# Kernel optimization log

Hardware: AMD Instinct MI355X
Metric: run time of the kernel (lower is better)

Reference implementation:

```python
import jax, jax.numpy as jnp
import numpy as np

B, S, D, H = 4, 2048, 1024, 16
HD = D // H  # head dim = 64

def setup_inputs() -> dict:
    key = jax.random.key(0)
    ks = jax.random.split(key, 6)
    scale = 0.02
    x = jax.random.normal(ks[0], (B, S, D), dtype=jnp.float32)
    Wq = jax.random.normal(ks[1], (D, D), dtype=jnp.float32) * scale
    Wk = jax.random.normal(ks[2], (D, D), dtype=jnp.float32) * scale
    Wv = jax.random.normal(ks[3], (D, D), dtype=jnp.float32) * scale
    Wo = jax.random.normal(ks[4], (D, D), dtype=jnp.float32) * scale
    bo = jnp.zeros((D,), dtype=jnp.float32)
    return {"x": x, "Wq": Wq, "Wk": Wk, "Wv": Wv, "Wo": Wo, "bo": bo}

def reference(x, Wq, Wk, Wv, Wo, bo):
    b, s, d = x.shape
    h, hd = H, HD
    # project and split heads -> [b, h, s, hd]
    def split_heads(t):
        return t.reshape(b, s, h, hd).transpose(0, 2, 1, 3)
    q = split_heads(x @ Wq)
    k = split_heads(x @ Wk)
    v = split_heads(x @ Wv)
    # causal attention with full score matrix (faithful to the naive impl)
    scores = jnp.einsum('bhqd,bhkd->bhqk', q, k)
    causal = jnp.triu(jnp.ones((s, s), dtype=bool), k=1)  # True above diagonal
    scores = jnp.where(causal, -jnp.inf, scores)
    attn = jax.nn.softmax(scores / jnp.sqrt(jnp.float32(hd)), axis=-1)
    ctx = jnp.einsum('bhqk,bhkd->bhqd', attn, v)
    ctx = ctx.transpose(0, 2, 1, 3).reshape(b, s, d)
    return ctx @ Wo + bo
```

## Files before the change

### kernel.cpp

```cpp
#include <hip/hip_runtime.h>
#include <math.h>
#include <stdint.h>

typedef __bf16 bf16;
typedef bf16 bf16x2 __attribute__((ext_vector_type(2)));
typedef bf16 bf16x8 __attribute__((ext_vector_type(8)));
typedef float floatx4 __attribute__((ext_vector_type(4)));

static constexpr int Sq = 2048, Dm = 1024, Hh = 16, HDim = 64;

#define GAS __attribute__((address_space(1)))
#define LAS __attribute__((address_space(3)))

__device__ __forceinline__ void dma16(const void* g, void* l) {
    __builtin_amdgcn_global_load_lds((const GAS void*)g, (LAS void*)l, 16, 0, 0);
}

__device__ __forceinline__ uint32_t pk_bf16(float a, float b) {
    bf16x2 t;
    t[0] = (bf16)a;
    t[1] = (bf16)b;
    return __builtin_bit_cast(uint32_t, t);
}

__global__ __launch_bounds__(256)
void prep_all(const float* __restrict__ Wq, const float* __restrict__ Wk,
              const float* __restrict__ Wv, const float* __restrict__ Wo,
              bf16* __restrict__ Wt,
              const float* __restrict__ x, bf16* __restrict__ xb)
{
    const int t = threadIdx.x;
    if (blockIdx.z == 4) {
        const int b = blockIdx.y * 16 + blockIdx.x;
        const size_t base = ((size_t)b * 256 + t) * 8;
#pragma unroll
        for (int it = 0; it < 16; it++) {
            const size_t i = base + (size_t)it * 524288;
            float4 f0 = *(const float4*)(x + i);
            float4 f1 = *(const float4*)(x + i + 4);
            bf16x8 v;
            v[0]=(bf16)f0.x; v[1]=(bf16)f0.y; v[2]=(bf16)f0.z; v[3]=(bf16)f0.w;
            v[4]=(bf16)f1.x; v[5]=(bf16)f1.y; v[6]=(bf16)f1.z; v[7]=(bf16)f1.w;
            *(bf16x8*)(xb + i) = v;
        }
        return;
    }
    const int w = blockIdx.z;
    const float* W = (w == 0) ? Wq : (w == 1) ? Wk : (w == 2) ? Wv : Wo;
    bf16* dst = Wt + (size_t)w * 1024 * 1024;
    const int k0 = blockIdx.x * 64, n0 = blockIdx.y * 64;
    __shared__ uint32_t Tl[64][33];
    {
        const int c8 = (t & 7) * 8;
        const int kp = t >> 3;
        const float* r0 = W + (size_t)(k0 + 2 * kp) * 1024 + n0 + c8;
        const float* r1 = r0 + 1024;
        float4 a0 = *(const float4*)r0, a1 = *(const float4*)(r0 + 4);
        float4 b0 = *(const float4*)r1, b1 = *(const float4*)(r1 + 4);
        float ra[8] = {a0.x, a0.y, a0.z, a0.w, a1.x, a1.y, a1.z, a1.w};
        float rb[8] = {b0.x, b0.y, b0.z, b0.w, b1.x, b1.y, b1.z, b1.w};
#pragma unroll
        for (int j = 0; j < 8; j++)
            Tl[c8 + j][kp] = pk_bf16(ra[j], rb[j]);
    }
    __syncthreads();
    {
        const int c = t >> 2, dq = (t & 3) * 8;
        uint32_t d[8];
#pragma unroll
        for (int i = 0; i < 8; i++) d[i] = Tl[c][dq + i];
        uint32_t* o = (uint32_t*)(dst + (size_t)(n0 + c) * 1024 + k0 + dq * 2);
        *(uint4*)o       = make_uint4(d[0], d[1], d[2], d[3]);
        *(uint4*)(o + 4) = make_uint4(d[4], d[5], d[6], d[7]);
    }
}

template <int AMODE>
__global__ __launch_bounds__(256, 2)
void qkv_gemm(const float* __restrict__ x, const bf16* __restrict__ xb,
              const bf16* __restrict__ Wt,
              bf16* __restrict__ Qb, bf16* __restrict__ Kb, bf16* __restrict__ VT)
{
    const int zz = blockIdx.z;
    const bf16* Wsel = Wt + (size_t)zz * 1024 * 1024;

    __shared__ __align__(16) unsigned char smem[34816];
    bf16 (*As1)[64] = (bf16(*)[64])smem;
    bf16 (*As0)[72] = (bf16(*)[72])smem;
    bf16 (*Bs)[64]  = (bf16(*)[64])(smem + (AMODE ? 16384 : 18432));

    const int tid  = threadIdx.x;
    const int wave = tid >> 6, lane = tid & 63, quad = lane >> 4, l16 = lane & 15;
    const int bm = blockIdx.x * 128, bn = blockIdx.y * 128;
    const int wm = (wave >> 1) * 64, wn = (wave & 1) * 64;

    floatx4 acc[4][4];
#pragma unroll
    for (int i = 0; i < 4; i++)
#pragma unroll
        for (int j = 0; j < 4; j++) acc[i][j] = (floatx4){0.f, 0.f, 0.f, 0.f};

    for (int k0 = 0; k0 < 1024; k0 += 64) {
        __syncthreads();
#pragma unroll
        for (int i = 0; i < 4; i++) {
            const int row = wave * 32 + i * 8 + (lane >> 3);
            const int lb  = (lane & 7) ^ (row & 7);
            const bf16* g = Wsel + (size_t)(bn + row) * 1024 + k0 + lb * 8;
            dma16((const void*)g, (void*)&Bs[wave * 32 + i * 8][0]);
        }
        if (AMODE) {
#pragma unroll
            for (int i = 0; i < 4; i++) {
                const int row = wave * 32 + i * 8 + (lane >> 3);
                const int lb  = (lane & 7) ^ (row & 7);
                const bf16* g = xb + (size_t)(bm + row) * 1024 + k0 + lb * 8;
                dma16((const void*)g, (void*)&As1[wave * 32 + i * 8][0]);
            }
        } else {
#pragma unroll
            for (int it = 0; it < 2; it++) {
                const int r  = (tid >> 2) + it * 64;
                const int cq = (tid & 3) * 16;
                const float* src = x + (size_t)(bm + r) * 1024 + k0 + cq;
                float4 f0 = *(const float4*)src,       f1 = *(const float4*)(src + 4);
                float4 f2 = *(const float4*)(src + 8), f3 = *(const float4*)(src + 12);
                bf16x8 v0, v1;
                v0[0]=(bf16)f0.x; v0[1]=(bf16)f0.y; v0[2]=(bf16)f0.z; v0[3]=(bf16)f0.w;
                v0[4]=(bf16)f1.x; v0[5]=(bf16)f1.y; v0[6]=(bf16)f1.z; v0[7]=(bf16)f1.w;
                v1[0]=(bf16)f2.x; v1[1]=(bf16)f2.y; v1[2]=(bf16)f2.z; v1[3]=(bf16)f2.w;
                v1[4]=(bf16)f3.x; v1[5]=(bf16)f3.y; v1[6]=(bf16)f3.z; v1[7]=(bf16)f3.w;
                *(bf16x8*)&As0[r][cq]     = v0;
                *(bf16x8*)&As0[r][cq + 8] = v1;
            }
        }
        __syncthreads();

#pragma unroll
        for (int kk = 0; kk < 2; kk++) {
            bf16x8 a[4], b[4];
#pragma unroll
            for (int tm = 0; tm < 4; tm++) {
                const int m = wm + tm * 16 + l16;
                if (AMODE) {
                    const int phys = (kk * 4 + quad) ^ (m & 7);
                    a[tm] = *(const bf16x8*)&As1[m][phys * 8];
                } else {
                    a[tm] = *(const bf16x8*)&As0[m][kk * 32 + quad * 8];
                }
            }
#pragma unroll
            for (int tn = 0; tn < 4; tn++) {
                const int n = wn + tn * 16 + l16;
                const int phys = (kk * 4 + quad) ^ (n & 7);
                b[tn] = *(const bf16x8*)&Bs[n][phys * 8];
            }
#pragma unroll
            for (int tm = 0; tm < 4; tm++)
#pragma unroll
                for (int tn = 0; tn < 4; tn++)
                    acc[tm][tn] = __builtin_amdgcn_mfma_f32_16x16x32_bf16(a[tm], b[tn], acc[tm][tn], 0, 0, 0);
        }
    }

    if (zz < 2) {
        bf16* dst = (zz == 0) ? Qb : Kb;
        const float sc = (zz == 1) ? 0.18033688f : 1.0f;
#pragma unroll
        for (int tm = 0; tm < 4; tm++)
#pragma unroll
            for (int tn = 0; tn < 4; tn++)
#pragma unroll
                for (int r = 0; r < 4; r++) {
                    const int m = bm + wm + tm * 16 + quad * 4 + r;
                    const int n = bn + wn + tn * 16 + l16;
                    const int bb = m >> 11, s = m & 2047;
                    const int h = n >> 6, d = n & 63;
                    dst[(((size_t)(bb * Hh + h)) * Sq + s) * HDim + d] = (bf16)(acc[tm][tn][r] * sc);
                }
    } else {
        __syncthreads();
        bf16 (*CT)[136] = (bf16(*)[136])smem;
#pragma unroll
        for (int tm = 0; tm < 4; tm++)
#pragma unroll
            for (int tn = 0; tn < 4; tn++)
#pragma unroll
                for (int r = 0; r < 4; r++) {
                    const int ml = wm + tm * 16 + quad * 4 + r;
                    const int nl = wn + tn * 16 + l16;
                    CT[nl][ml] = (bf16)acc[tm][tn][r];
                }
        __syncthreads();
        const int nl = tid >> 1, part = tid & 1;
        const int n = bn + nl, h = n >> 6, d = n & 63;
        const int bbv = bm >> 11, s0v = bm & 2047;
        bf16* o = VT + (((size_t)(bbv * Hh + h)) * HDim + d) * Sq + s0v + part * 64;
#pragma unroll
        for (int i = 0; i < 8; i++)
            *(bf16x8*)(o + i * 8) = *(const bf16x8*)&CT[nl][part * 64 + i * 8];
    }
}

__global__ __launch_bounds__(128)
void attn(const bf16* __restrict__ Qb, const bf16* __restrict__ Kb,
          const bf16* __restrict__ VTg, bf16* __restrict__ Cx)
{
    const int bh = blockIdx.x;
    const int bl = bh >> 4, h = bh & 15;

    __shared__ __align__(16) bf16 Kl[2][64][64];
    __shared__ __align__(16) bf16 Vt[2][64][64];
    __shared__ __align__(16) bf16 PlT[2][32][64];

    const int tid  = threadIdx.x;
    const int wave = tid >> 6, lane = tid & 63, quad = lane >> 4, l16 = lane & 15;

    const int srow = wave * 32 + (lane >> 3);
    const int lb   = (lane & 7) ^ (lane >> 3);

    for (int pass = 0; pass < 2; pass++) {
        const int qt = (pass == 0) ? (int)blockIdx.y : 31 - (int)blockIdx.y;
        const int q0 = qt * 64 + wave * 32;
        const int nk = qt + 1;

        bf16x8 bq[2][2];
#pragma unroll
        for (int nt = 0; nt < 2; nt++) {
            const bf16* Qrow = Qb + ((size_t)bh * Sq + q0 + nt * 16 + l16) * HDim;
            bq[nt][0] = *(const bf16x8*)(Qrow + quad * 8);
            bq[nt][1] = *(const bf16x8*)(Qrow + 32 + quad * 8);
        }

        floatx4 acc[4][2];
#pragma unroll
        for (int i = 0; i < 4; i++)
#pragma unroll
            for (int j = 0; j < 2; j++) acc[i][j] = (floatx4){0.f, 0.f, 0.f, 0.f};
        float l_part[2] = {0.f, 0.f};

        const bf16* kp = Kb  + ((size_t)bh * Sq + srow) * HDim + lb * 8;
        const bf16* vp = VTg + ((size_t)bh * HDim + srow) * Sq + lb * 8;

        auto stage = [&](int nb) {
#pragma unroll
            for (int i = 0; i < 4; i++) {
                dma16((const void*)(kp + (size_t)(i * 8) * HDim), (void*)&Kl[nb][wave * 32 + i * 8][0]);
                dma16((const void*)(vp + (size_t)(i * 8) * Sq),  (void*)&Vt[nb][wave * 32 + i * 8][0]);
            }
            kp += 64 * HDim;
            vp += 64;
        };

        auto tile = [&](int nb, bool masked) {
            const bf16 (*Ksm)[64] = Kl[nb];
            const bf16 (*Vsm)[64] = Vt[nb];

            floatx4 sT[4][2];
            __builtin_amdgcn_s_setprio(1);
#pragma unroll
            for (int mt = 0; mt < 4; mt++) {
                const int kr = mt * 16 + l16;
                bf16x8 ak0 = *(const bf16x8*)&Ksm[kr][(quad ^ (kr & 7)) * 8];
                bf16x8 ak1 = *(const bf16x8*)&Ksm[kr][((4 + quad) ^ (kr & 7)) * 8];
#pragma unroll
                for (int nt = 0; nt < 2; nt++) {
                    floatx4 z = (floatx4){0.f, 0.f, 0.f, 0.f};
                    z = __builtin_amdgcn_mfma_f32_16x16x32_bf16(ak0, bq[nt][0], z, 0, 0, 0);
                    z = __builtin_amdgcn_mfma_f32_16x16x32_bf16(ak1, bq[nt][1], z, 0, 0, 0);
                    sT[mt][nt] = z;
                }
            }
            __builtin_amdgcn_s_setprio(0);

            if (masked) {
#pragma unroll
                for (int mt = 0; mt < 4; mt++)
#pragma unroll
                    for (int nt = 0; nt < 2; nt++)
#pragma unroll
                        for (int r = 0; r < 4; r++) {
                            const int keyl  = mt * 16 + quad * 4 + r;
                            const int qrowl = wave * 32 + nt * 16 + l16;
                            if (keyl > qrowl) sT[mt][nt][r] = -1e30f;
                        }
            }

#pragma unroll
            for (int nt = 0; nt < 2; nt++) {
                float rs = 0.f;
#pragma unroll
                for (int mt = 0; mt < 4; mt++)
#pragma unroll
                    for (int r = 0; r < 4; r++) {
                        const float e = __builtin_amdgcn_exp2f(sT[mt][nt][r]);
                        sT[mt][nt][r] = e;
                        rs += e;
                    }
                l_part[nt] += rs;
            }

#pragma unroll
            for (int mt = 0; mt < 4; mt++)
#pragma unroll
                for (int nt = 0; nt < 2; nt++) {
                    uint2 pk;
                    pk.x = pk_bf16(sT[mt][nt][0], sT[mt][nt][1]);
                    pk.y = pk_bf16(sT[mt][nt][2], sT[mt][nt][3]);
                    const int row  = nt * 16 + l16;
                    const int boff = (mt * 32 + quad * 8) ^ ((row & 7) << 4);
                    *(uint2*)((char*)&PlT[wave][row][0] + boff) = pk;
                }

#pragma unroll
            for (int ks = 0; ks < 2; ks++) {
                bf16x8 bp[2];
#pragma unroll
                for (int nt = 0; nt < 2; nt++) {
                    const int row  = nt * 16 + l16;
                    const int boff = (ks * 64 + quad * 16) ^ ((row & 7) << 4);
                    bp[nt] = *(const bf16x8*)((const char*)&PlT[wave][row][0] + boff);
                }
                __builtin_amdgcn_s_setprio(1);
#pragma unroll
                for (int mt = 0; mt < 4; mt++) {
                    const int vr = mt * 16 + l16;
                    bf16x8 av = *(const bf16x8*)&Vsm[vr][((ks * 4 + quad) ^ (vr & 7)) * 8];
#pragma unroll
                    for (int nt = 0; nt < 2; nt++)
                        acc[mt][nt] = __builtin_amdgcn_mfma_f32_16x16x32_bf16(av, bp[nt], acc[mt][nt], 0, 0, 0);
                }
                __builtin_amdgcn_s_setprio(0);
            }
        };

        stage(0);
        for (int kt = 0; kt < nk - 1; kt++) {
            const int cur = kt & 1;
            stage(cur ^ 1);
            asm volatile("s_waitcnt vmcnt(8)" ::: "memory");
            __builtin_amdgcn_s_barrier();
            tile(cur, false);
            __builtin_amdgcn_s_barrier();
        }
        asm volatile("s_waitcnt vmcnt(0)" ::: "memory");
        __builtin_amdgcn_s_barrier();
        tile((nk - 1) & 1, true);
        __builtin_amdgcn_s_barrier();

#pragma unroll
        for (int nt = 0; nt < 2; nt++) {
            float rs = l_part[nt];
            rs += __shfl_xor(rs, 16, 64);
            rs += __shfl_xor(rs, 32, 64);
            const float inv = __builtin_amdgcn_rcpf(rs);
            const int qrow = q0 + nt * 16 + l16;
#pragma unroll
            for (int mt = 0; mt < 4; mt++) {
                uint2 pk;
                pk.x = pk_bf16(acc[mt][nt][0] * inv, acc[mt][nt][1] * inv);
                pk.y = pk_bf16(acc[mt][nt][2] * inv, acc[mt][nt][3] * inv);
                *(uint2*)(Cx + ((size_t)(bl * Sq + qrow)) * Dm + h * HDim + mt * 16 + quad * 4) = pk;
            }
        }
    }
}

__global__ __launch_bounds__(256, 2)
void out_gemm(const bf16* __restrict__ Cx, const bf16* __restrict__ WtO,
              const float* __restrict__ bo, float* __restrict__ out, int mbase)
{
    __shared__ __align__(16) bf16 As2[128][64];
    __shared__ __align__(16) bf16 Bs2[128][64];

    const int tid  = threadIdx.x;
    const int wave = tid >> 6, lane = tid & 63, quad = lane >> 4, l16 = lane & 15;
    const int bm = blockIdx.x * 128, bn = blockIdx.y * 128;
    const int wm = (wave >> 1) * 64, wn = (wave & 1) * 64;

    floatx4 acc[4][4];
#pragma unroll
    for (int i = 0; i < 4; i++)
#pragma unroll
        for (int j = 0; j < 4; j++) acc[i][j] = (floatx4){0.f, 0.f, 0.f, 0.f};

    for (int k0 = 0; k0 < 1024; k0 += 64) {
        __syncthreads();
#pragma unroll
        for (int i = 0; i < 4; i++) {
            const int row = wave * 32 + i * 8 + (lane >> 3);
            const int lb  = (lane & 7) ^ (row & 7);
            const bf16* ga = Cx  + (size_t)(bm + row) * 1024 + k0 + lb * 8;
            const bf16* gb = WtO + (size_t)(bn + row) * 1024 + k0 + lb * 8;
            dma16((const void*)ga, (void*)&As2[wave * 32 + i * 8][0]);
            dma16((const void*)gb, (void*)&Bs2[wave * 32 + i * 8][0]);
        }
        __syncthreads();

#pragma unroll
        for (int kk = 0; kk < 2; kk++) {
            bf16x8 a[4], b[4];
#pragma unroll
            for (int tm = 0; tm < 4; tm++) {
                const int m = wm + tm * 16 + l16;
                const int phys = (kk * 4 + quad) ^ (m & 7);
                a[tm] = *(const bf16x8*)&As2[m][phys * 8];
            }
#pragma unroll
            for (int tn = 0; tn < 4; tn++) {
                const int n = wn + tn * 16 + l16;
                const int phys = (kk * 4 + quad) ^ (n & 7);
                b[tn] = *(const bf16x8*)&Bs2[n][phys * 8];
            }
#pragma unroll
            for (int tm = 0; tm < 4; tm++)
#pragma unroll
                for (int tn = 0; tn < 4; tn++)
                    acc[tm][tn] = __builtin_amdgcn_mfma_f32_16x16x32_bf16(a[tm], b[tn], acc[tm][tn], 0, 0, 0);
        }
    }

#pragma unroll
    for (int tm = 0; tm < 4; tm++)
#pragma unroll
        for (int tn = 0; tn < 4; tn++)
#pragma unroll
            for (int r = 0; r < 4; r++) {
                const int m = bm + wm + tm * 16 + quad * 4 + r;
                const int n = bn + wn + tn * 16 + l16;
                out[(size_t)(mbase + m) * 1024 + n] = acc[tm][tn][r] + bo[n];
            }
}

extern "C" void kernel_launch(void* const* d_in, const int* in_sizes, int n_in,
                              void* d_out, int out_size, void* d_ws, size_t ws_size,
                              hipStream_t stream)
{
    const float* x  = (const float*)d_in[0];
    const float* Wq = (const float*)d_in[1];
    const float* Wk = (const float*)d_in[2];
    const float* Wv = (const float*)d_in[3];
    const float* Wo = (const float*)d_in[4];
    const float* bo = (const float*)d_in[5];
    float* out = (float*)d_out;

    const size_t M1 = 1024 * 1024;
    const size_t XE = (size_t)8192 * 1024;

    if (ws_size >= (size_t)72 * 1024 * 1024) {
        bf16* Wt = (bf16*)d_ws;
        bf16* xb = Wt + 4 * M1;
        bf16* Qb = xb + XE;
        bf16* Kb = Qb + XE;
        bf16* VT = Kb + XE;
        bf16* Cx = xb;

        prep_all<<<dim3(16, 16, 5), 256, 0, stream>>>(Wq, Wk, Wv, Wo, Wt, x, xb);
        qkv_gemm<1><<<dim3(64, 8, 3), 256, 0, stream>>>(x, xb, Wt, Qb, Kb, VT);
        attn<<<dim3(64, 16), 128, 0, stream>>>(Qb, Kb, VT, Cx);
        out_gemm<<<dim3(64, 8), 256, 0, stream>>>(Cx, Wt + 3 * M1, bo, out, 0);
    } else {
        bf16* Wt = (bf16*)d_ws;
        bf16* Qb = Wt + 4 * M1;
        bf16* Kb = Qb + XE;
        bf16* VT = Kb + XE;
        bf16* Cx = VT + XE;

        prep_all<<<dim3(16, 16, 4), 256, 0, stream>>>(Wq, Wk, Wv, Wo, Wt, nullptr, nullptr);
        qkv_gemm<0><<<dim3(64, 8, 3), 256, 0, stream>>>(x, nullptr, Wt, Qb, Kb, VT);
        const size_t chunk = (size_t)2 * Hh * Sq * HDim;
        for (int c = 0; c < 2; c++) {
            attn<<<dim3(32, 16), 128, 0, stream>>>(Qb + c * chunk, Kb + c * chunk,
                                                   VT + c * chunk, Cx);
            out_gemm<<<dim3(32, 8), 256, 0, stream>>>(Cx, Wt + 3 * M1, bo, out, c * 4096);
        }
    }
}
```

Measured before the change: 240.7 us.

## Split attention query tile across four waves of 16 rows each

The attention kernel now launches 256 threads per block, and each of four waves handles 16 query rows instead of two waves handling 32. K/V staging is spread over four waves with half the DMA per wave, and the wait count is adjusted to match. The goal is more waves in flight and lower register pressure per wave, to hide latency better. In exchange, each wave gets less reuse of the K/V fragments it reads from LDS per MFMA, and there are more barrier participants.

```diff
diff --git a/kernel.cpp b/kernel.cpp
--- a/kernel.cpp
+++ b/kernel.cpp
@@ -202,7 +202,7 @@
     }
 }
 
-__global__ __launch_bounds__(128)
+__global__ __launch_bounds__(256, 4)
 void attn(const bf16* __restrict__ Qb, const bf16* __restrict__ Kb,
           const bf16* __restrict__ VTg, bf16* __restrict__ Cx)
 {
@@ -211,42 +211,39 @@
 
     __shared__ __align__(16) bf16 Kl[2][64][64];
     __shared__ __align__(16) bf16 Vt[2][64][64];
-    __shared__ __align__(16) bf16 PlT[2][32][64];
+    __shared__ __align__(16) bf16 PlT[4][16][64];
 
     const int tid  = threadIdx.x;
     const int wave = tid >> 6, lane = tid & 63, quad = lane >> 4, l16 = lane & 15;
 
-    const int srow = wave * 32 + (lane >> 3);
+    const int srow = wave * 16 + (lane >> 3);
     const int lb   = (lane & 7) ^ (lane >> 3);
 
     for (int pass = 0; pass < 2; pass++) {
         const int qt = (pass == 0) ? (int)blockIdx.y : 31 - (int)blockIdx.y;
-        const int q0 = qt * 64 + wave * 32;
+        const int q0 = qt * 64;
         const int nk = qt + 1;
 
-        bf16x8 bq[2][2];
-#pragma unroll
-        for (int nt = 0; nt < 2; nt++) {
-            const bf16* Qrow = Qb + ((size_t)bh * Sq + q0 + nt * 16 + l16) * HDim;
-            bq[nt][0] = *(const bf16x8*)(Qrow + quad * 8);
-            bq[nt][1] = *(const bf16x8*)(Qrow + 32 + quad * 8);
-        }
-
-        floatx4 acc[4][2];
-#pragma unroll
-        for (int i = 0; i < 4; i++)
-#pragma unroll
-            for (int j = 0; j < 2; j++) acc[i][j] = (floatx4){0.f, 0.f, 0.f, 0.f};
-        float l_part[2] = {0.f, 0.f};
+        bf16x8 bq[2];
+        {
+            const bf16* Qrow = Qb + ((size_t)bh * Sq + q0 + wave * 16 + l16) * HDim;
+            bq[0] = *(const bf16x8*)(Qrow + quad * 8);
+            bq[1] = *(const bf16x8*)(Qrow + 32 + quad * 8);
+        }
+
+        floatx4 acc[4];
+#pragma unroll
+        for (int i = 0; i < 4; i++) acc[i] = (floatx4){0.f, 0.f, 0.f, 0.f};
+        float l_part = 0.f;
 
         const bf16* kp = Kb  + ((size_t)bh * Sq + srow) * HDim + lb * 8;
         const bf16* vp = VTg + ((size_t)bh * HDim + srow) * Sq + lb * 8;
 
         auto stage = [&](int nb) {
 #pragma unroll
-            for (int i = 0; i < 4; i++) {
-                dma16((const void*)(kp + (size_t)(i * 8) * HDim), (void*)&Kl[nb][wave * 32 + i * 8][0]);
-                dma16((const void*)(vp + (size_t)(i * 8) * Sq),  (void*)&Vt[nb][wave * 32 + i * 8][0]);
+            for (int i = 0; i < 2; i++) {
+                dma16((const void*)(kp + (size_t)(i * 8) * HDim), (void*)&Kl[nb][wave * 16 + i * 8][0]);
+                dma16((const void*)(vp + (size_t)(i * 8) * Sq),  (void*)&Vt[nb][wave * 16 + i * 8][0]);
             }
             kp += 64 * HDim;
             vp += 64;
@@ -256,20 +253,17 @@
             const bf16 (*Ksm)[64] = Kl[nb];
             const bf16 (*Vsm)[64] = Vt[nb];
 
-            floatx4 sT[4][2];
+            floatx4 sT[4];
             __builtin_amdgcn_s_setprio(1);
 #pragma unroll
             for (int mt = 0; mt < 4; mt++) {
                 const int kr = mt * 16 + l16;
                 bf16x8 ak0 = *(const bf16x8*)&Ksm[kr][(quad ^ (kr & 7)) * 8];
                 bf16x8 ak1 = *(const bf16x8*)&Ksm[kr][((4 + quad) ^ (kr & 7)) * 8];
-#pragma unroll
-                for (int nt = 0; nt < 2; nt++) {
-                    floatx4 z = (floatx4){0.f, 0.f, 0.f, 0.f};
-                    z = __builtin_amdgcn_mfma_f32_16x16x32_bf16(ak0, bq[nt][0], z, 0, 0, 0);
-                    z = __builtin_amdgcn_mfma_f32_16x16x32_bf16(ak1, bq[nt][1], z, 0, 0, 0);
-                    sT[mt][nt] = z;
-                }
+                floatx4 z = (floatx4){0.f, 0.f, 0.f, 0.f};
+                z = __builtin_amdgcn_mfma_f32_16x16x32_bf16(ak0, bq[0], z, 0, 0, 0);
+                z = __builtin_amdgcn_mfma_f32_16x16x32_bf16(ak1, bq[1], z, 0, 0, 0);
+                sT[mt] = z;
             }
             __builtin_amdgcn_s_setprio(0);
 
@@ -277,58 +271,45 @@
 #pragma unroll
                 for (int mt = 0; mt < 4; mt++)
 #pragma unroll
-                    for (int nt = 0; nt < 2; nt++)
-#pragma unroll
-                        for (int r = 0; r < 4; r++) {
-                            const int keyl  = mt * 16 + quad * 4 + r;
-                            const int qrowl = wave * 32 + nt * 16 + l16;
-                            if (keyl > qrowl) sT[mt][nt][r] = -1e30f;
-                        }
-            }
-
-#pragma unroll
-            for (int nt = 0; nt < 2; nt++) {
+                    for (int r = 0; r < 4; r++) {
+                        const int keyl  = mt * 16 + quad * 4 + r;
+                        const int qrowl = wave * 16 + l16;
+                        if (keyl > qrowl) sT[mt][r] = -1e30f;
+                    }
+            }
+
+            {
                 float rs = 0.f;
 #pragma unroll
                 for (int mt = 0; mt < 4; mt++)
 #pragma unroll
                     for (int r = 0; r < 4; r++) {
-                        const float e = __builtin_amdgcn_exp2f(sT[mt][nt][r]);
-                        sT[mt][nt][r] = e;
+                        const float e = __builtin_amdgcn_exp2f(sT[mt][r]);
+                        sT[mt][r] = e;
                         rs += e;
                     }
-                l_part[nt] += rs;
-            }
-
-#pragma unroll
-            for (int mt = 0; mt < 4; mt++)
-#pragma unroll
-                for (int nt = 0; nt < 2; nt++) {
-                    uint2 pk;
-                    pk.x = pk_bf16(sT[mt][nt][0], sT[mt][nt][1]);
-                    pk.y = pk_bf16(sT[mt][nt][2], sT[mt][nt][3]);
-                    const int row  = nt * 16 + l16;
-                    const int boff = (mt * 32 + quad * 8) ^ ((row & 7) << 4);
-                    *(uint2*)((char*)&PlT[wave][row][0] + boff) = pk;
-                }
+                l_part += rs;
+            }
+
+#pragma unroll
+            for (int mt = 0; mt < 4; mt++) {
+                uint2 pk;
+                pk.x = pk_bf16(sT[mt][0], sT[mt][1]);
+                pk.y = pk_bf16(sT[mt][2], sT[mt][3]);
+                const int boff = (mt * 32 + quad * 8) ^ ((l16 & 7) << 4);
+                *(uint2*)((char*)&PlT[wave][l16][0] + boff) = pk;
+            }
 
 #pragma unroll
             for (int ks = 0; ks < 2; ks++) {
-                bf16x8 bp[2];
-#pragma unroll
-                for (int nt = 0; nt < 2; nt++) {
-                    const int row  = nt * 16 + l16;
-                    const int boff = (ks * 64 + quad * 16) ^ ((row & 7) << 4);
-                    bp[nt] = *(const bf16x8*)((const char*)&PlT[wave][row][0] + boff);
-                }
+                const int boff = (ks * 64 + quad * 16) ^ ((l16 & 7) << 4);
+                bf16x8 bp = *(const bf16x8*)((const char*)&PlT[wave][l16][0] + boff);
                 __builtin_amdgcn_s_setprio(1);
 #pragma unroll
                 for (int mt = 0; mt < 4; mt++) {
                     const int vr = mt * 16 + l16;
                     bf16x8 av = *(const bf16x8*)&Vsm[vr][((ks * 4 + quad) ^ (vr & 7)) * 8];
-#pragma unroll
-                    for (int nt = 0; nt < 2; nt++)
-                        acc[mt][nt] = __builtin_amdgcn_mfma_f32_16x16x32_bf16(av, bp[nt], acc[mt][nt], 0, 0, 0);
+                    acc[mt] = __builtin_amdgcn_mfma_f32_16x16x32_bf16(av, bp, acc[mt], 0, 0, 0);
                 }
                 __builtin_amdgcn_s_setprio(0);
             }
@@ -338,7 +319,7 @@
         for (int kt = 0; kt < nk - 1; kt++) {
             const int cur = kt & 1;
             stage(cur ^ 1);
-            asm volatile("s_waitcnt vmcnt(8)" ::: "memory");
+            asm volatile("s_waitcnt vmcnt(4)" ::: "memory");
             __builtin_amdgcn_s_barrier();
             tile(cur, false);
             __builtin_amdgcn_s_barrier();
@@ -348,18 +329,17 @@
         tile((nk - 1) & 1, true);
         __builtin_amdgcn_s_barrier();
 
-#pragma unroll
-        for (int nt = 0; nt < 2; nt++) {
-            float rs = l_part[nt];
+        {
+            float rs = l_part;
             rs += __shfl_xor(rs, 16, 64);
             rs += __shfl_xor(rs, 32, 64);
             const float inv = __builtin_amdgcn_rcpf(rs);
-            const int qrow = q0 + nt * 16 + l16;
+            const int qrow = q0 + wave * 16 + l16;
 #pragma unroll
             for (int mt = 0; mt < 4; mt++) {
                 uint2 pk;
-                pk.x = pk_bf16(acc[mt][nt][0] * inv, acc[mt][nt][1] * inv);
-                pk.y = pk_bf16(acc[mt][nt][2] * inv, acc[mt][nt][3] * inv);
+                pk.x = pk_bf16(acc[mt][0] * inv, acc[mt][1] * inv);
+                pk.y = pk_bf16(acc[mt][2] * inv, acc[mt][3] * inv);
                 *(uint2*)(Cx + ((size_t)(bl * Sq + qrow)) * Dm + h * HDim + mt * 16 + quad * 4) = pk;
             }
         }
@@ -457,7 +437,7 @@
 
         prep_all<<<dim3(16, 16, 5), 256, 0, stream>>>(Wq, Wk, Wv, Wo, Wt, x, xb);
         qkv_gemm<1><<<dim3(64, 8, 3), 256, 0, stream>>>(x, xb, Wt, Qb, Kb, VT);
-        attn<<<dim3(64, 16), 128, 0, stream>>>(Qb, Kb, VT, Cx);
+        attn<<<dim3(64, 16), 256, 0, stream>>>(Qb, Kb, VT, Cx);
         out_gemm<<<dim3(64, 8), 256, 0, stream>>>(Cx, Wt + 3 * M1, bo, out, 0);
     } else {
         bf16* Wt = (bf16*)d_ws;
@@ -470,7 +450,7 @@
         qkv_gemm<0><<<dim3(64, 8, 3), 256, 0, stream>>>(x, nullptr, Wt, Qb, Kb, VT);
         const size_t chunk = (size_t)2 * Hh * Sq * HDim;
         for (int c = 0; c < 2; c++) {
-            attn<<<dim3(32, 16), 128, 0, stream>>>(Qb + c * chunk, Kb + c * chunk,
+            attn<<<dim3(32, 16), 256, 0, stream>>>(Qb + c * chunk, Kb + c * chunk,
                                                    VT + c * chunk, Cx);
             out_gemm<<<dim3(32, 8), 256, 0, stream>>>(Cx, Wt + 3 * M1, bo, out, c * 4096);
         }
```

Result: faster. 234.3 us (-2.7%).

## Split attention key tiles across four waves with LDS cross-wave reduction

Applied to the files above, without the earlier changes.

The attention kernel now runs 256 threads per block with one 64-row query tile per block, no longer pairing two tiles per 128-thread block. Each wave takes 16 keys of every 64-key tile for all 64 queries, keeps P in registers as a zero-padded MFMA operand so the LDS round trip for P goes away, and the partial outputs are reduced across waves through LDS at the end. This gives more waves per CU and removes the per-tile P staging, but it adds a multi-barrier epilogue reduction, wastes half of each PV MFMA on zero padding, and drops the causal load balancing that pairing tiles provided.

```diff
diff --git a/kernel.cpp b/kernel.cpp
--- a/kernel.cpp
+++ b/kernel.cpp
@@ -202,167 +202,168 @@
     }
 }
 
-__global__ __launch_bounds__(128)
+__global__ __launch_bounds__(256, 3)
 void attn(const bf16* __restrict__ Qb, const bf16* __restrict__ Kb,
           const bf16* __restrict__ VTg, bf16* __restrict__ Cx)
 {
     const int bh = blockIdx.x;
     const int bl = bh >> 4, h = bh & 15;
-
-    __shared__ __align__(16) bf16 Kl[2][64][64];
-    __shared__ __align__(16) bf16 Vt[2][64][64];
-    __shared__ __align__(16) bf16 PlT[2][32][64];
+    const int qt = 31 - (int)blockIdx.y;
+    const int q0 = qt * 64;
+    const int nk = qt + 1;
+
+    __shared__ __align__(16) char smem[33792];
+    bf16 (*Kl)[64][64] = (bf16(*)[64][64])smem;
+    bf16 (*Vt)[64][64] = (bf16(*)[64][64])(smem + 16384);
+    float (*Rq)[64][20] = (float(*)[64][20])smem;
+    float (*Lred)[4][16] = (float(*)[4][16])(smem + 32768);
 
     const int tid  = threadIdx.x;
     const int wave = tid >> 6, lane = tid & 63, quad = lane >> 4, l16 = lane & 15;
 
-    const int srow = wave * 32 + (lane >> 3);
+    const int srow = wave * 16 + (lane >> 3);
     const int lb   = (lane & 7) ^ (lane >> 3);
 
-    for (int pass = 0; pass < 2; pass++) {
-        const int qt = (pass == 0) ? (int)blockIdx.y : 31 - (int)blockIdx.y;
-        const int q0 = qt * 64 + wave * 32;
-        const int nk = qt + 1;
-
-        bf16x8 bq[2][2];
-#pragma unroll
-        for (int nt = 0; nt < 2; nt++) {
-            const bf16* Qrow = Qb + ((size_t)bh * Sq + q0 + nt * 16 + l16) * HDim;
-            bq[nt][0] = *(const bf16x8*)(Qrow + quad * 8);
-            bq[nt][1] = *(const bf16x8*)(Qrow + 32 + quad * 8);
-        }
-
-        floatx4 acc[4][2];
-#pragma unroll
-        for (int i = 0; i < 4; i++)
-#pragma unroll
-            for (int j = 0; j < 2; j++) acc[i][j] = (floatx4){0.f, 0.f, 0.f, 0.f};
-        float l_part[2] = {0.f, 0.f};
-
-        const bf16* kp = Kb  + ((size_t)bh * Sq + srow) * HDim + lb * 8;
-        const bf16* vp = VTg + ((size_t)bh * HDim + srow) * Sq + lb * 8;
-
-        auto stage = [&](int nb) {
-#pragma unroll
-            for (int i = 0; i < 4; i++) {
-                dma16((const void*)(kp + (size_t)(i * 8) * HDim), (void*)&Kl[nb][wave * 32 + i * 8][0]);
-                dma16((const void*)(vp + (size_t)(i * 8) * Sq),  (void*)&Vt[nb][wave * 32 + i * 8][0]);
-            }
-            kp += 64 * HDim;
-            vp += 64;
-        };
-
-        auto tile = [&](int nb, bool masked) {
-            const bf16 (*Ksm)[64] = Kl[nb];
-            const bf16 (*Vsm)[64] = Vt[nb];
-
-            floatx4 sT[4][2];
+    bf16x8 bq[4][2];
+#pragma unroll
+    for (int nt = 0; nt < 4; nt++) {
+        const bf16* Qrow = Qb + ((size_t)bh * Sq + q0 + nt * 16 + l16) * HDim;
+        bq[nt][0] = *(const bf16x8*)(Qrow + quad * 8);
+        bq[nt][1] = *(const bf16x8*)(Qrow + 32 + quad * 8);
+    }
+
+    floatx4 acc[4][4];
+#pragma unroll
+    for (int i = 0; i < 4; i++)
+#pragma unroll
+        for (int j = 0; j < 4; j++) acc[i][j] = (floatx4){0.f, 0.f, 0.f, 0.f};
+    float l_part[4] = {0.f, 0.f, 0.f, 0.f};
+
+    const bf16* kp = Kb  + ((size_t)bh * Sq + srow) * HDim + lb * 8;
+    const bf16* vp = VTg + ((size_t)bh * HDim + srow) * Sq + lb * 8;
+
+    auto stage = [&](int nb) {
+#pragma unroll
+        for (int i = 0; i < 2; i++) {
+            dma16((const void*)(kp + (size_t)(i * 8) * HDim), (void*)&Kl[nb][wave * 16 + i * 8][0]);
+            dma16((const void*)(vp + (size_t)(i * 8) * Sq),  (void*)&Vt[nb][wave * 16 + i * 8][0]);
+        }
+        kp += 64 * HDim;
+        vp += 64;
+    };
+
+    auto tile = [&](int nb, bool masked) {
+        const bf16 (*Ksm)[64] = Kl[nb];
+        const bf16 (*Vsm)[64] = Vt[nb];
+
+        const int kr = wave * 16 + l16;
+        const bf16x8 ak0 = *(const bf16x8*)&Ksm[kr][(quad ^ (kr & 7)) * 8];
+        const bf16x8 ak1 = *(const bf16x8*)&Ksm[kr][((4 + quad) ^ (kr & 7)) * 8];
+
+        bf16x8 pb[4];
+#pragma unroll
+        for (int nt = 0; nt < 4; nt++) {
+            floatx4 z = (floatx4){0.f, 0.f, 0.f, 0.f};
             __builtin_amdgcn_s_setprio(1);
-#pragma unroll
-            for (int mt = 0; mt < 4; mt++) {
-                const int kr = mt * 16 + l16;
-                bf16x8 ak0 = *(const bf16x8*)&Ksm[kr][(quad ^ (kr & 7)) * 8];
-                bf16x8 ak1 = *(const bf16x8*)&Ksm[kr][((4 + quad) ^ (kr & 7)) * 8];
-#pragma unroll
-                for (int nt = 0; nt < 2; nt++) {
-                    floatx4 z = (floatx4){0.f, 0.f, 0.f, 0.f};
-                    z = __builtin_amdgcn_mfma_f32_16x16x32_bf16(ak0, bq[nt][0], z, 0, 0, 0);
-                    z = __builtin_amdgcn_mfma_f32_16x16x32_bf16(ak1, bq[nt][1], z, 0, 0, 0);
-                    sT[mt][nt] = z;
+            z = __builtin_amdgcn_mfma_f32_16x16x32_bf16(ak0, bq[nt][0], z, 0, 0, 0);
+            z = __builtin_amdgcn_mfma_f32_16x16x32_bf16(ak1, bq[nt][1], z, 0, 0, 0);
+            __builtin_amdgcn_s_setprio(0);
+            if (masked) {
+#pragma unroll
+                for (int r = 0; r < 4; r++) {
+                    const int keyl = wave * 16 + quad * 4 + r;
+                    if (keyl > nt * 16 + l16) z[r] = -1e30f;
                 }
             }
+            float rs = 0.f;
+#pragma unroll
+            for (int r = 0; r < 4; r++) {
+                const float e = __builtin_amdgcn_exp2f(z[r]);
+                z[r] = e;
+                rs += e;
+            }
+            l_part[nt] += rs;
+            const uint32_t p0 = pk_bf16(z[0], z[1]);
+            const uint32_t p1 = pk_bf16(z[2], z[3]);
+            pb[nt] = __builtin_bit_cast(bf16x8, make_uint4(p0, p1, 0u, 0u));
+        }
+
+#pragma unroll
+        for (int j = 0; j < 4; j++) {
+            const int row = ((wave + j) & 3) * 16 + l16;
+            const int sl  = ((wave * 2 + (quad >> 1)) ^ (row & 7)) * 16 + (quad & 1) * 8;
+            const uint2 v = *(const uint2*)((const char*)&Vsm[row][0] + sl);
+            const bf16x8 av = __builtin_bit_cast(bf16x8, make_uint4(v.x, v.y, 0u, 0u));
+            __builtin_amdgcn_s_setprio(1);
+#pragma unroll
+            for (int nt = 0; nt < 4; nt++)
+                acc[j][nt] = __builtin_amdgcn_mfma_f32_16x16x32_bf16(av, pb[nt], acc[j][nt], 0, 0, 0);
             __builtin_amdgcn_s_setprio(0);
-
-            if (masked) {
-#pragma unroll
-                for (int mt = 0; mt < 4; mt++)
-#pragma unroll
-                    for (int nt = 0; nt < 2; nt++)
-#pragma unroll
-                        for (int r = 0; r < 4; r++) {
-                            const int keyl  = mt * 16 + quad * 4 + r;
-                            const int qrowl = wave * 32 + nt * 16 + l16;
-                            if (keyl > qrowl) sT[mt][nt][r] = -1e30f;
-                        }
-            }
-
-#pragma unroll
-            for (int nt = 0; nt < 2; nt++) {
-                float rs = 0.f;
-#pragma unroll
-                for (int mt = 0; mt < 4; mt++)
-#pragma unroll
-                    for (int r = 0; r < 4; r++) {
-                        const float e = __builtin_amdgcn_exp2f(sT[mt][nt][r]);
-                        sT[mt][nt][r] = e;
-                        rs += e;
-                    }
-                l_part[nt] += rs;
-            }
-
-#pragma unroll
-            for (int mt = 0; mt < 4; mt++)
-#pragma unroll
-                for (int nt = 0; nt < 2; nt++) {
-                    uint2 pk;
-                    pk.x = pk_bf16(sT[mt][nt][0], sT[mt][nt][1]);
-                    pk.y = pk_bf16(sT[mt][nt][2], sT[mt][nt][3]);
-                    const int row  = nt * 16 + l16;
-                    const int boff = (mt * 32 + quad * 8) ^ ((row & 7) << 4);
-                    *(uint2*)((char*)&PlT[wave][row][0] + boff) = pk;
-                }
-
-#pragma unroll
-            for (int ks = 0; ks < 2; ks++) {
-                bf16x8 bp[2];
-#pragma unroll
-                for (int nt = 0; nt < 2; nt++) {
-                    const int row  = nt * 16 + l16;
-                    const int boff = (ks * 64 + quad * 16) ^ ((row & 7) << 4);
-                    bp[nt] = *(const bf16x8*)((const char*)&PlT[wave][row][0] + boff);
-                }
-                __builtin_amdgcn_s_setprio(1);
-#pragma unroll
-                for (int mt = 0; mt < 4; mt++) {
-                    const int vr = mt * 16 + l16;
-                    bf16x8 av = *(const bf16x8*)&Vsm[vr][((ks * 4 + quad) ^ (vr & 7)) * 8];
-#pragma unroll
-                    for (int nt = 0; nt < 2; nt++)
-                        acc[mt][nt] = __builtin_amdgcn_mfma_f32_16x16x32_bf16(av, bp[nt], acc[mt][nt], 0, 0, 0);
-                }
-                __builtin_amdgcn_s_setprio(0);
-            }
-        };
-
-        stage(0);
-        for (int kt = 0; kt < nk - 1; kt++) {
-            const int cur = kt & 1;
-            stage(cur ^ 1);
-            asm volatile("s_waitcnt vmcnt(8)" ::: "memory");
-            __builtin_amdgcn_s_barrier();
-            tile(cur, false);
-            __builtin_amdgcn_s_barrier();
-        }
-        asm volatile("s_waitcnt vmcnt(0)" ::: "memory");
+        }
+    };
+
+    stage(0);
+    for (int kt = 0; kt < nk - 1; kt++) {
+        const int cur = kt & 1;
+        stage(cur ^ 1);
+        asm volatile("s_waitcnt vmcnt(4)" ::: "memory");
         __builtin_amdgcn_s_barrier();
-        tile((nk - 1) & 1, true);
+        tile(cur, false);
         __builtin_amdgcn_s_barrier();
-
-#pragma unroll
-        for (int nt = 0; nt < 2; nt++) {
-            float rs = l_part[nt];
-            rs += __shfl_xor(rs, 16, 64);
-            rs += __shfl_xor(rs, 32, 64);
-            const float inv = __builtin_amdgcn_rcpf(rs);
-            const int qrow = q0 + nt * 16 + l16;
-#pragma unroll
-            for (int mt = 0; mt < 4; mt++) {
-                uint2 pk;
-                pk.x = pk_bf16(acc[mt][nt][0] * inv, acc[mt][nt][1] * inv);
-                pk.y = pk_bf16(acc[mt][nt][2] * inv, acc[mt][nt][3] * inv);
-                *(uint2*)(Cx + ((size_t)(bl * Sq + qrow)) * Dm + h * HDim + mt * 16 + quad * 4) = pk;
-            }
-        }
+    }
+    asm volatile("s_waitcnt vmcnt(0)" ::: "memory");
+    __builtin_amdgcn_s_barrier();
+    tile((nk - 1) & 1, true);
+
+    float lw[4];
+#pragma unroll
+    for (int nt = 0; nt < 4; nt++) {
+        float rs = l_part[nt];
+        rs += __shfl_xor(rs, 16, 64);
+        rs += __shfl_xor(rs, 32, 64);
+        lw[nt] = rs;
+    }
+    __syncthreads();
+    if (quad == 0) {
+#pragma unroll
+        for (int nt = 0; nt < 4; nt++) Lred[wave][nt][l16] = lw[nt];
+    }
+#pragma unroll
+    for (int nt = 0; nt < 4; nt++)
+        *(floatx4*)&Rq[wave][nt * 16 + l16][quad * 4] = acc[1][nt];
+    __syncthreads();
+    float lsum[4];
+#pragma unroll
+    for (int nt = 0; nt < 4; nt++)
+        lsum[nt] = Lred[0][nt][l16] + Lred[1][nt][l16] + Lred[2][nt][l16] + Lred[3][nt][l16];
+#pragma unroll
+    for (int nt = 0; nt < 4; nt++)
+        acc[0][nt] += *(const floatx4*)&Rq[(wave + 3) & 3][nt * 16 + l16][quad * 4];
+    __syncthreads();
+#pragma unroll
+    for (int nt = 0; nt < 4; nt++)
+        *(floatx4*)&Rq[wave][nt * 16 + l16][quad * 4] = acc[2][nt];
+    __syncthreads();
+#pragma unroll
+    for (int nt = 0; nt < 4; nt++)
+        acc[0][nt] += *(const floatx4*)&Rq[(wave + 2) & 3][nt * 16 + l16][quad * 4];
+    __syncthreads();
+#pragma unroll
+    for (int nt = 0; nt < 4; nt++)
+        *(floatx4*)&Rq[wave][nt * 16 + l16][quad * 4] = acc[3][nt];
+    __syncthreads();
+#pragma unroll
+    for (int nt = 0; nt < 4; nt++)
+        acc[0][nt] += *(const floatx4*)&Rq[(wave + 1) & 3][nt * 16 + l16][quad * 4];
+
+#pragma unroll
+    for (int nt = 0; nt < 4; nt++) {
+        const float inv = __builtin_amdgcn_rcpf(lsum[nt]);
+        uint2 pk;
+        pk.x = pk_bf16(acc[0][nt][0] * inv, acc[0][nt][1] * inv);
+        pk.y = pk_bf16(acc[0][nt][2] * inv, acc[0][nt][3] * inv);
+        const int qrow = q0 + nt * 16 + l16;
+        *(uint2*)(Cx + ((size_t)(bl * Sq + qrow)) * Dm + h * HDim + wave * 16 + quad * 4) = pk;
     }
 }
 
@@ -457,7 +458,7 @@
 
         prep_all<<<dim3(16, 16, 5), 256, 0, stream>>>(Wq, Wk, Wv, Wo, Wt, x, xb);
         qkv_gemm<1><<<dim3(64, 8, 3), 256, 0, stream>>>(x, xb, Wt, Qb, Kb, VT);
-        attn<<<dim3(64, 16), 128, 0, stream>>>(Qb, Kb, VT, Cx);
+        attn<<<dim3(64, 32), 256, 0, stream>>>(Qb, Kb, VT, Cx);
         out_gemm<<<dim3(64, 8), 256, 0, stream>>>(Cx, Wt + 3 * M1, bo, out, 0);
     } else {
         bf16* Wt = (bf16*)d_ws;
@@ -470,7 +471,7 @@
         qkv_gemm<0><<<dim3(64, 8, 3), 256, 0, stream>>>(x, nullptr, Wt, Qb, Kb, VT);
         const size_t chunk = (size_t)2 * Hh * Sq * HDim;
         for (int c = 0; c < 2; c++) {
-            attn<<<dim3(32, 16), 128, 0, stream>>>(Qb + c * chunk, Kb + c * chunk,
+            attn<<<dim3(32, 32), 256, 0, stream>>>(Qb + c * chunk, Kb + c * chunk,
                                                    VT + c * chunk, Cx);
             out_gemm<<<dim3(32, 8), 256, 0, stream>>>(Cx, Wt + 3 * M1, bo, out, c * 4096);
         }
```

After: 238.2 us. About the same (-1.1%).
